# Kernel tuning notes

Measured on AMD Instinct MI355X. Metric: run time of the kernel, lower is better.

## Reference

```python
import jax, jax.numpy as jnp
import numpy as np

D_MODEL, D_K, D_V, N_HEADS = 1024, 64, 64, 16
B, S = 4, 2048


def setup_inputs() -> dict:
    key = jax.random.key(0)
    ks = jax.random.split(key, 11)
    sd = 0.02
    return {
        "q": jax.random.normal(ks[0], (B, S, D_MODEL), jnp.float32),
        "k": jax.random.normal(ks[1], (B, S, D_MODEL), jnp.float32),
        "v": jax.random.normal(ks[2], (B, S, D_MODEL), jnp.float32),
        # stacked per-head projection weights (equivalent to n_heads separate nn.Linear)
        "Wq": jax.random.normal(ks[3], (N_HEADS, D_MODEL, D_K), jnp.float32) * sd,
        "bq": jax.random.normal(ks[4], (N_HEADS, D_K), jnp.float32) * sd,
        "Wk": jax.random.normal(ks[5], (N_HEADS, D_MODEL, D_K), jnp.float32) * sd,
        "bk": jax.random.normal(ks[6], (N_HEADS, D_K), jnp.float32) * sd,
        "Wv": jax.random.normal(ks[7], (N_HEADS, D_MODEL, D_V), jnp.float32) * sd,
        "bv": jax.random.normal(ks[8], (N_HEADS, D_V), jnp.float32) * sd,
        "Wo": jax.random.normal(ks[9], (N_HEADS * D_V, D_MODEL), jnp.float32) * sd,
        "bo": jax.random.normal(ks[10], (D_MODEL,), jnp.float32) * sd,
    }


def reference(q, k, v, Wq, bq, Wk, bk, Wv, bv, Wo, bo):
    # Per-head projections, batched over heads: (B,S,D) x (H,D,dk) -> (B,H,S,dk)
    qh = jnp.einsum("bsd,hdk->bhsk", q, Wq) + bq[None, :, None, :]
    kh = jnp.einsum("bsd,hdk->bhsk", k, Wk) + bk[None, :, None, :]
    vh = jnp.einsum("bsd,hdk->bhsk", v, Wv) + bv[None, :, None, :]
    # scaled dot-product attention per head
    scores = jnp.einsum("bhqk,bhsk->bhqs", qh, kh) / jnp.sqrt(jnp.float32(D_K))
    attn = jax.nn.softmax(scores, axis=-1)
    ctx = jnp.einsum("bhqs,bhsv->bhqv", attn, vh)  # (B,H,S,dv)
    # concat heads -> (B,S,H*dv), then output projection
    ctx = jnp.transpose(ctx, (0, 2, 1, 3)).reshape(B, S, N_HEADS * D_V)
    return ctx @ Wo + bo
```

## Files before the change

### kernel.cpp

```cpp
#include <hip/hip_runtime.h>
#include <hip/hip_bf16.h>

#define DM 1024
#define SEQ 2048
#define NB 4
#define NH 16
#define DKV 64

typedef unsigned short u16;
typedef unsigned int u32;
typedef __attribute__((ext_vector_type(8))) short bf16x8;
typedef __attribute__((ext_vector_type(4))) float f32x4;

__device__ __forceinline__ u16 f2bf(float f) {
    union { float f; unsigned u; } x; x.f = f;
    unsigned r = x.u + 0x7fffu + ((x.u >> 16) & 1u);
    return (u16)(r >> 16);
}
__device__ __forceinline__ u16 f2bf1(float f) {
    union { float f; unsigned u; } x; x.f = f;
    return (u16)((x.u + 0x8000u) >> 16);
}
__device__ __forceinline__ u32 pack2bf(float a, float b) {
    union { float f; unsigned u; } xa, xb; xa.f = a; xb.f = b;
    return __builtin_amdgcn_perm(xb.u + 0x8000u, xa.u + 0x8000u, 0x07060302);
}

#define GLDS16(gp, lp) __builtin_amdgcn_global_load_lds( \
    (const __attribute__((address_space(1))) u32*)(const void*)(gp), \
    (__attribute__((address_space(3))) u32*)(void*)(lp), 16, 0, 0)

__global__ __launch_bounds__(256)
void transpose_to_bf16(const float* __restrict__ src, u16* __restrict__ dst,
                       int R, int C, long srcHeadStride, long dstHeadStride) {
    int h = blockIdx.z;
    src += (long)h * srcHeadStride;
    dst += (long)h * dstHeadStride;
    __shared__ float tile[32][33];
    int r0 = blockIdx.y * 32, c0 = blockIdx.x * 32;
    int tc = threadIdx.x & 31, tr = threadIdx.x >> 5;
    for (int j = 0; j < 4; j++) {
        int r = tr + j * 8;
        tile[r][tc] = src[(long)(r0 + r) * C + c0 + tc];
    }
    __syncthreads();
    for (int j = 0; j < 4; j++) {
        int rr = tr + j * 8;
        dst[(long)(c0 + rr) * R + r0 + tc] = f2bf(tile[tc][rr]);
    }
}

__global__ __launch_bounds__(256)
void cvt_f32_bf16(const float* __restrict__ src, u16* __restrict__ dst, int n4) {
    int i = blockIdx.x * 256 + threadIdx.x;
    int stride = gridDim.x * 256;
    for (; i < n4; i += stride) {
        float4 v = ((const float4*)src)[i];
        uint2 o; o.x = pack2bf(v.x, v.y); o.y = pack2bf(v.z, v.w);
        ((uint2*)dst)[i] = o;
    }
}

template<int OUTMODE>
__global__ __launch_bounds__(256)
void gemm_bf16(const u16* __restrict__ A, const u16* __restrict__ Bt,
               const float* __restrict__ bias, void* __restrict__ Cptr) {
    const int bm0 = blockIdx.x * 128;
    const int bn0 = blockIdx.y * 128;
    __shared__ __align__(16) u16 AsL[128 * 64];
    __shared__ __align__(16) u16 BsL[128 * 64];
    const int tid = threadIdx.x;
    const int lane = tid & 63;
    const int wave = tid >> 6;
    const int wm = (wave >> 1) * 64, wn = (wave & 1) * 64;
    const int l15 = lane & 15, quad = lane >> 4;

    f32x4 acc[4][4];
    for (int i = 0; i < 4; i++) for (int j = 0; j < 4; j++) acc[i][j] = (f32x4)0.0f;

    int rr[4], cc[4];
    for (int j = 0; j < 4; j++) {
        int ci = (wave * 4 + j) * 64 + lane;
        rr[j] = ci >> 3;
        cc[j] = (ci & 7) ^ (rr[j] & 7);
    }
    const int swz = l15 & 7;

    for (int kk = 0; kk < DM; kk += 64) {
        for (int j = 0; j < 4; j++)
            GLDS16(A + (size_t)(bm0 + rr[j]) * DM + kk + cc[j] * 8, AsL + (wave * 4 + j) * 512);
        for (int j = 0; j < 4; j++)
            GLDS16(Bt + (size_t)(bn0 + rr[j]) * DM + kk + cc[j] * 8, BsL + (wave * 4 + j) * 512);
        __syncthreads();
        for (int ks = 0; ks < 2; ks++) {
            bf16x8 a[4], b[4];
            const int fo = ((ks * 4 + quad) ^ swz) * 8;
            for (int mi = 0; mi < 4; mi++)
                a[mi] = *(const bf16x8*)&AsL[(wm + mi * 16 + l15) * 64 + fo];
            for (int ni = 0; ni < 4; ni++)
                b[ni] = *(const bf16x8*)&BsL[(wn + ni * 16 + l15) * 64 + fo];
            for (int mi = 0; mi < 4; mi++)
                for (int ni = 0; ni < 4; ni++)
                    acc[mi][ni] = __builtin_amdgcn_mfma_f32_16x16x32_bf16(a[mi], b[ni], acc[mi][ni], 0, 0, 0);
        }
        __syncthreads();
    }
    for (int mi = 0; mi < 4; mi++) {
        for (int ni = 0; ni < 4; ni++) {
            int n = bn0 + wn + ni * 16 + l15;
            float bb = bias[n];
            int m0 = bm0 + wm + mi * 16 + quad * 4;
            float v0 = acc[mi][ni][0] + bb, v1 = acc[mi][ni][1] + bb;
            float v2 = acc[mi][ni][2] + bb, v3 = acc[mi][ni][3] + bb;
            if (OUTMODE == 0) {
                float* C = (float*)Cptr;
                C[(size_t)(m0 + 0) * DM + n] = v0;
                C[(size_t)(m0 + 1) * DM + n] = v1;
                C[(size_t)(m0 + 2) * DM + n] = v2;
                C[(size_t)(m0 + 3) * DM + n] = v3;
            } else if (OUTMODE == 1) {
                u16* C = (u16*)Cptr;
                int b = m0 >> 11, s = m0 & 2047;
                int h = n >> 6, d = n & 63;
                size_t base = (((size_t)(b * NH + h)) * SEQ + s) * DKV + d;
                C[base + 0 * DKV] = f2bf1(v0);
                C[base + 1 * DKV] = f2bf1(v1);
                C[base + 2 * DKV] = f2bf1(v2);
                C[base + 3 * DKV] = f2bf1(v3);
            } else {
                u16* C = (u16*)Cptr;
                int b = m0 >> 11, s = m0 & 2047;
                int h = n >> 6, d = n & 63;
                uint2 pk; pk.x = pack2bf(v0, v1); pk.y = pack2bf(v2, v3);
                *(uint2*)&C[(((size_t)(b * NH + h)) * DKV + d) * SEQ + s] = pk;
            }
        }
    }
}

__global__ __launch_bounds__(256)
void attn_kernel(const u16* __restrict__ qh, const u16* __restrict__ kh,
                 const u16* __restrict__ vt, u16* __restrict__ ctx) {
    const int qblk = blockIdx.x;
    const int h = blockIdx.y;
    const int b = blockIdx.z;
    const int tid = threadIdx.x;
    const int lane = tid & 63;
    const int wave = tid >> 6;
    const int l15 = lane & 15, quad = lane >> 4;
    const size_t headoff = ((size_t)(b * NH + h)) * SEQ * DKV;
    const u16* Q = qh + headoff;
    const u16* K = kh + headoff;
    const u16* V = vt + headoff;
    const int q0 = qblk * 128 + wave * 32;

    __shared__ __align__(16) u16 KsL[64 * 64];
    __shared__ __align__(16) u16 VtL[64 * 64];
    __shared__ __align__(16) u16 Ps[4][32][80];

    bf16x8 aq[2][2];
    for (int ni = 0; ni < 2; ni++)
        for (int ks = 0; ks < 2; ks++)
            aq[ni][ks] = *(const bf16x8*)&Q[(size_t)(q0 + ni * 16 + l15) * DKV + ks * 32 + quad * 8];

    f32x4 ot[4][2];
    for (int di = 0; di < 4; di++) for (int ni = 0; ni < 2; ni++) ot[di][ni] = (f32x4)0.0f;
    float l_[2] = {0.0f, 0.0f};

    const float sc = 0.125f * 1.44269504088896f;

    int rr[2], cc[2];
    for (int j = 0; j < 2; j++) {
        int ci = (wave * 2 + j) * 64 + lane;
        rr[j] = ci >> 3;
        cc[j] = (ci & 7) ^ (rr[j] & 7);
    }
    const int swz = l15 & 7;

    for (int kv0 = 0; kv0 < SEQ; kv0 += 64) {
        for (int j = 0; j < 2; j++) {
            GLDS16(K + (size_t)(kv0 + rr[j]) * DKV + cc[j] * 8, KsL + (wave * 2 + j) * 512);
            GLDS16(V + (size_t)rr[j] * SEQ + kv0 + cc[j] * 8, VtL + (wave * 2 + j) * 512);
        }
        __syncthreads();

        f32x4 st[4][2];
        for (int mi = 0; mi < 4; mi++) for (int ni = 0; ni < 2; ni++) st[mi][ni] = (f32x4)0.0f;
        for (int ks = 0; ks < 2; ks++) {
            const int fo = ((ks * 4 + quad) ^ swz) * 8;
            bf16x8 bk[4];
            for (int mi = 0; mi < 4; mi++)
                bk[mi] = *(const bf16x8*)&KsL[(mi * 16 + l15) * 64 + fo];
            for (int mi = 0; mi < 4; mi++)
                for (int ni = 0; ni < 2; ni++)
                    st[mi][ni] = __builtin_amdgcn_mfma_f32_16x16x32_bf16(bk[mi], aq[ni][ks], st[mi][ni], 0, 0, 0);
        }

        for (int ni = 0; ni < 2; ni++) {
            float rs = 0.0f;
            for (int mi = 0; mi < 4; mi++) {
                f32x4 p;
                p.x = exp2f(st[mi][ni].x * sc);
                p.y = exp2f(st[mi][ni].y * sc);
                p.z = exp2f(st[mi][ni].z * sc);
                p.w = exp2f(st[mi][ni].w * sc);
                rs += (p.x + p.y) + (p.z + p.w);
                uint2 pk; pk.x = pack2bf(p.x, p.y); pk.y = pack2bf(p.z, p.w);
                *(uint2*)&Ps[wave][ni * 16 + l15][mi * 16 + quad * 4] = pk;
            }
            rs += __shfl_xor(rs, 16);
            rs += __shfl_xor(rs, 32);
            l_[ni] += rs;
        }
        __threadfence_block();

        for (int ks = 0; ks < 2; ks++) {
            const int fo = ((ks * 4 + quad) ^ swz) * 8;
            bf16x8 av[4], bp[2];
            for (int di = 0; di < 4; di++)
                av[di] = *(const bf16x8*)&VtL[(di * 16 + l15) * 64 + fo];
            for (int ni = 0; ni < 2; ni++)
                bp[ni] = *(const bf16x8*)&Ps[wave][ni * 16 + l15][ks * 32 + quad * 8];
            for (int di = 0; di < 4; di++)
                for (int ni = 0; ni < 2; ni++)
                    ot[di][ni] = __builtin_amdgcn_mfma_f32_16x16x32_bf16(av[di], bp[ni], ot[di][ni], 0, 0, 0);
        }
        __syncthreads();
    }

    for (int ni = 0; ni < 2; ni++) {
        float inv = 1.0f / l_[ni];
        int srow = q0 + ni * 16 + l15;
        for (int di = 0; di < 4; di++) {
            uint2 pk;
            pk.x = pack2bf(ot[di][ni].x * inv, ot[di][ni].y * inv);
            pk.y = pack2bf(ot[di][ni].z * inv, ot[di][ni].w * inv);
            *(uint2*)&ctx[((size_t)b * SEQ + srow) * DM + h * DKV + di * 16 + quad * 4] = pk;
        }
    }
}

extern "C" void kernel_launch(void* const* d_in, const int* in_sizes, int n_in,
                              void* d_out, int out_size, void* d_ws, size_t ws_size,
                              hipStream_t stream) {
    const float* q  = (const float*)d_in[0];
    const float* k  = (const float*)d_in[1];
    const float* v  = (const float*)d_in[2];
    const float* Wq = (const float*)d_in[3];
    const float* bq = (const float*)d_in[4];
    const float* Wk = (const float*)d_in[5];
    const float* bk = (const float*)d_in[6];
    const float* Wv = (const float*)d_in[7];
    const float* bv = (const float*)d_in[8];
    const float* Wo = (const float*)d_in[9];
    const float* bo = (const float*)d_in[10];
    float* out = (float*)d_out;

    char* ws = (char*)d_ws;
    const size_t MB = 1024 * 1024;
    u16* WqT = (u16*)(ws + 0 * MB);
    u16* WkT = (u16*)(ws + 2 * MB);
    u16* WvT = (u16*)(ws + 4 * MB);
    u16* WoT = (u16*)(ws + 6 * MB);
    u16* qh  = (u16*)(ws + 8 * MB);
    u16* kh  = (u16*)(ws + 24 * MB);
    u16* vh  = (u16*)(ws + 40 * MB);
    u16* ctx = (u16*)(ws + 56 * MB);
    u16* cvt = ctx;

    const int n4 = NB * SEQ * DM / 4;

    transpose_to_bf16<<<dim3(2, 32, 16), 256, 0, stream>>>(Wq, WqT, 1024, 64, 1024 * 64, 64 * 1024);
    transpose_to_bf16<<<dim3(2, 32, 16), 256, 0, stream>>>(Wk, WkT, 1024, 64, 1024 * 64, 64 * 1024);
    transpose_to_bf16<<<dim3(2, 32, 16), 256, 0, stream>>>(Wv, WvT, 1024, 64, 1024 * 64, 64 * 1024);
    transpose_to_bf16<<<dim3(32, 32, 1), 256, 0, stream>>>(Wo, WoT, 1024, 1024, 0, 0);

    cvt_f32_bf16<<<dim3(2048), 256, 0, stream>>>(q, cvt, n4);
    gemm_bf16<1><<<dim3(64, 8), 256, 0, stream>>>(cvt, WqT, bq, qh);
    cvt_f32_bf16<<<dim3(2048), 256, 0, stream>>>(k, cvt, n4);
    gemm_bf16<1><<<dim3(64, 8), 256, 0, stream>>>(cvt, WkT, bk, kh);
    cvt_f32_bf16<<<dim3(2048), 256, 0, stream>>>(v, cvt, n4);
    gemm_bf16<2><<<dim3(64, 8), 256, 0, stream>>>(cvt, WvT, bv, vh);

    attn_kernel<<<dim3(16, 16, 4), 256, 0, stream>>>(qh, kh, vh, ctx);

    gemm_bf16<0><<<dim3(64, 8), 256, 0, stream>>>(ctx, WoT, bo, out);
}
```

Measured before the change: 408.9 us.

## Double-buffer LDS tiles, fold softmax scale into Q, compute row sums via MFMA

Both the projection GEMM and the attention kernel now use two LDS buffers, prefetching the next K-tile while the current one is computed, which removes one barrier per iteration. The softmax scale times log2(e) is applied in the Q projection epilogue, so the attention loop no longer multiplies scores. Row sums of P come from an extra MFMA against a vector of bf16 ones instead of shuffle reductions, and the P scratch padding shrinks. The costs are doubled LDS use, which may lower occupancy, and row sums taken from bf16-rounded P rather than fp32 values.

```diff
diff --git a/kernel.cpp b/kernel.cpp
--- a/kernel.cpp
+++ b/kernel.cpp
@@ -64,11 +64,11 @@
 template<int OUTMODE>
 __global__ __launch_bounds__(256)
 void gemm_bf16(const u16* __restrict__ A, const u16* __restrict__ Bt,
-               const float* __restrict__ bias, void* __restrict__ Cptr) {
+               const float* __restrict__ bias, void* __restrict__ Cptr, float cscale) {
     const int bm0 = blockIdx.x * 128;
     const int bn0 = blockIdx.y * 128;
-    __shared__ __align__(16) u16 AsL[128 * 64];
-    __shared__ __align__(16) u16 BsL[128 * 64];
+    __shared__ __align__(16) u16 AsL[2][128 * 64];
+    __shared__ __align__(16) u16 BsL[2][128 * 64];
     const int tid = threadIdx.x;
     const int lane = tid & 63;
     const int wave = tid >> 6;
@@ -86,32 +86,40 @@
     }
     const int swz = l15 & 7;
 
+    for (int j = 0; j < 4; j++)
+        GLDS16(A + (size_t)(bm0 + rr[j]) * DM + cc[j] * 8, &AsL[0][(wave * 4 + j) * 512]);
+    for (int j = 0; j < 4; j++)
+        GLDS16(Bt + (size_t)(bn0 + rr[j]) * DM + cc[j] * 8, &BsL[0][(wave * 4 + j) * 512]);
+
+    int buf = 0;
     for (int kk = 0; kk < DM; kk += 64) {
-        for (int j = 0; j < 4; j++)
-            GLDS16(A + (size_t)(bm0 + rr[j]) * DM + kk + cc[j] * 8, AsL + (wave * 4 + j) * 512);
-        for (int j = 0; j < 4; j++)
-            GLDS16(Bt + (size_t)(bn0 + rr[j]) * DM + kk + cc[j] * 8, BsL + (wave * 4 + j) * 512);
         __syncthreads();
+        if (kk + 64 < DM) {
+            for (int j = 0; j < 4; j++)
+                GLDS16(A + (size_t)(bm0 + rr[j]) * DM + kk + 64 + cc[j] * 8, &AsL[buf ^ 1][(wave * 4 + j) * 512]);
+            for (int j = 0; j < 4; j++)
+                GLDS16(Bt + (size_t)(bn0 + rr[j]) * DM + kk + 64 + cc[j] * 8, &BsL[buf ^ 1][(wave * 4 + j) * 512]);
+        }
         for (int ks = 0; ks < 2; ks++) {
             bf16x8 a[4], b[4];
             const int fo = ((ks * 4 + quad) ^ swz) * 8;
             for (int mi = 0; mi < 4; mi++)
-                a[mi] = *(const bf16x8*)&AsL[(wm + mi * 16 + l15) * 64 + fo];
+                a[mi] = *(const bf16x8*)&AsL[buf][(wm + mi * 16 + l15) * 64 + fo];
             for (int ni = 0; ni < 4; ni++)
-                b[ni] = *(const bf16x8*)&BsL[(wn + ni * 16 + l15) * 64 + fo];
+                b[ni] = *(const bf16x8*)&BsL[buf][(wn + ni * 16 + l15) * 64 + fo];
             for (int mi = 0; mi < 4; mi++)
                 for (int ni = 0; ni < 4; ni++)
                     acc[mi][ni] = __builtin_amdgcn_mfma_f32_16x16x32_bf16(a[mi], b[ni], acc[mi][ni], 0, 0, 0);
         }
-        __syncthreads();
+        buf ^= 1;
     }
     for (int mi = 0; mi < 4; mi++) {
         for (int ni = 0; ni < 4; ni++) {
             int n = bn0 + wn + ni * 16 + l15;
             float bb = bias[n];
             int m0 = bm0 + wm + mi * 16 + quad * 4;
-            float v0 = acc[mi][ni][0] + bb, v1 = acc[mi][ni][1] + bb;
-            float v2 = acc[mi][ni][2] + bb, v3 = acc[mi][ni][3] + bb;
+            float v0 = (acc[mi][ni][0] + bb) * cscale, v1 = (acc[mi][ni][1] + bb) * cscale;
+            float v2 = (acc[mi][ni][2] + bb) * cscale, v3 = (acc[mi][ni][3] + bb) * cscale;
             if (OUTMODE == 0) {
                 float* C = (float*)Cptr;
                 C[(size_t)(m0 + 0) * DM + n] = v0;
@@ -154,20 +162,22 @@
     const u16* V = vt + headoff;
     const int q0 = qblk * 128 + wave * 32;
 
-    __shared__ __align__(16) u16 KsL[64 * 64];
-    __shared__ __align__(16) u16 VtL[64 * 64];
-    __shared__ __align__(16) u16 Ps[4][32][80];
+    __shared__ __align__(16) u16 KsL[2][64 * 64];
+    __shared__ __align__(16) u16 VtL[2][64 * 64];
+    __shared__ __align__(16) u16 Ps[4][32][72];
 
     bf16x8 aq[2][2];
     for (int ni = 0; ni < 2; ni++)
         for (int ks = 0; ks < 2; ks++)
             aq[ni][ks] = *(const bf16x8*)&Q[(size_t)(q0 + ni * 16 + l15) * DKV + ks * 32 + quad * 8];
 
+    bf16x8 vones;
+    for (int j = 0; j < 8; j++) vones[j] = (short)0x3F80;
+
     f32x4 ot[4][2];
     for (int di = 0; di < 4; di++) for (int ni = 0; ni < 2; ni++) ot[di][ni] = (f32x4)0.0f;
-    float l_[2] = {0.0f, 0.0f};
-
-    const float sc = 0.125f * 1.44269504088896f;
+    f32x4 lacc[2];
+    lacc[0] = (f32x4)0.0f; lacc[1] = (f32x4)0.0f;
 
     int rr[2], cc[2];
     for (int j = 0; j < 2; j++) {
@@ -177,12 +187,21 @@
     }
     const int swz = l15 & 7;
 
+    for (int j = 0; j < 2; j++) {
+        GLDS16(K + (size_t)rr[j] * DKV + cc[j] * 8, &KsL[0][(wave * 2 + j) * 512]);
+        GLDS16(V + (size_t)rr[j] * SEQ + cc[j] * 8, &VtL[0][(wave * 2 + j) * 512]);
+    }
+
+    int buf = 0;
     for (int kv0 = 0; kv0 < SEQ; kv0 += 64) {
-        for (int j = 0; j < 2; j++) {
-            GLDS16(K + (size_t)(kv0 + rr[j]) * DKV + cc[j] * 8, KsL + (wave * 2 + j) * 512);
-            GLDS16(V + (size_t)rr[j] * SEQ + kv0 + cc[j] * 8, VtL + (wave * 2 + j) * 512);
-        }
         __syncthreads();
+        if (kv0 + 64 < SEQ) {
+            int nx = kv0 + 64;
+            for (int j = 0; j < 2; j++) {
+                GLDS16(K + (size_t)(nx + rr[j]) * DKV + cc[j] * 8, &KsL[buf ^ 1][(wave * 2 + j) * 512]);
+                GLDS16(V + (size_t)rr[j] * SEQ + nx + cc[j] * 8, &VtL[buf ^ 1][(wave * 2 + j) * 512]);
+            }
+        }
 
         f32x4 st[4][2];
         for (int mi = 0; mi < 4; mi++) for (int ni = 0; ni < 2; ni++) st[mi][ni] = (f32x4)0.0f;
@@ -190,27 +209,22 @@
             const int fo = ((ks * 4 + quad) ^ swz) * 8;
             bf16x8 bk[4];
             for (int mi = 0; mi < 4; mi++)
-                bk[mi] = *(const bf16x8*)&KsL[(mi * 16 + l15) * 64 + fo];
+                bk[mi] = *(const bf16x8*)&KsL[buf][(mi * 16 + l15) * 64 + fo];
             for (int mi = 0; mi < 4; mi++)
                 for (int ni = 0; ni < 2; ni++)
                     st[mi][ni] = __builtin_amdgcn_mfma_f32_16x16x32_bf16(bk[mi], aq[ni][ks], st[mi][ni], 0, 0, 0);
         }
 
         for (int ni = 0; ni < 2; ni++) {
-            float rs = 0.0f;
             for (int mi = 0; mi < 4; mi++) {
                 f32x4 p;
-                p.x = exp2f(st[mi][ni].x * sc);
-                p.y = exp2f(st[mi][ni].y * sc);
-                p.z = exp2f(st[mi][ni].z * sc);
-                p.w = exp2f(st[mi][ni].w * sc);
-                rs += (p.x + p.y) + (p.z + p.w);
+                p.x = exp2f(st[mi][ni].x);
+                p.y = exp2f(st[mi][ni].y);
+                p.z = exp2f(st[mi][ni].z);
+                p.w = exp2f(st[mi][ni].w);
                 uint2 pk; pk.x = pack2bf(p.x, p.y); pk.y = pack2bf(p.z, p.w);
                 *(uint2*)&Ps[wave][ni * 16 + l15][mi * 16 + quad * 4] = pk;
             }
-            rs += __shfl_xor(rs, 16);
-            rs += __shfl_xor(rs, 32);
-            l_[ni] += rs;
         }
         __threadfence_block();
 
@@ -218,18 +232,20 @@
             const int fo = ((ks * 4 + quad) ^ swz) * 8;
             bf16x8 av[4], bp[2];
             for (int di = 0; di < 4; di++)
-                av[di] = *(const bf16x8*)&VtL[(di * 16 + l15) * 64 + fo];
+                av[di] = *(const bf16x8*)&VtL[buf][(di * 16 + l15) * 64 + fo];
             for (int ni = 0; ni < 2; ni++)
                 bp[ni] = *(const bf16x8*)&Ps[wave][ni * 16 + l15][ks * 32 + quad * 8];
             for (int di = 0; di < 4; di++)
                 for (int ni = 0; ni < 2; ni++)
                     ot[di][ni] = __builtin_amdgcn_mfma_f32_16x16x32_bf16(av[di], bp[ni], ot[di][ni], 0, 0, 0);
-        }
-        __syncthreads();
+            for (int ni = 0; ni < 2; ni++)
+                lacc[ni] = __builtin_amdgcn_mfma_f32_16x16x32_bf16(vones, bp[ni], lacc[ni], 0, 0, 0);
+        }
+        buf ^= 1;
     }
 
     for (int ni = 0; ni < 2; ni++) {
-        float inv = 1.0f / l_[ni];
+        float inv = 1.0f / lacc[ni][0];
         int srow = q0 + ni * 16 + l15;
         for (int di = 0; di < 4; di++) {
             uint2 pk;
@@ -269,6 +285,7 @@
     u16* cvt = ctx;
 
     const int n4 = NB * SEQ * DM / 4;
+    const float SC = 0.125f * 1.44269504088896f;
 
     transpose_to_bf16<<<dim3(2, 32, 16), 256, 0, stream>>>(Wq, WqT, 1024, 64, 1024 * 64, 64 * 1024);
     transpose_to_bf16<<<dim3(2, 32, 16), 256, 0, stream>>>(Wk, WkT, 1024, 64, 1024 * 64, 64 * 1024);
@@ -276,13 +293,13 @@
     transpose_to_bf16<<<dim3(32, 32, 1), 256, 0, stream>>>(Wo, WoT, 1024, 1024, 0, 0);
 
     cvt_f32_bf16<<<dim3(2048), 256, 0, stream>>>(q, cvt, n4);
-    gemm_bf16<1><<<dim3(64, 8), 256, 0, stream>>>(cvt, WqT, bq, qh);
+    gemm_bf16<1><<<dim3(64, 8), 256, 0, stream>>>(cvt, WqT, bq, qh, SC);
     cvt_f32_bf16<<<dim3(2048), 256, 0, stream>>>(k, cvt, n4);
-    gemm_bf16<1><<<dim3(64, 8), 256, 0, stream>>>(cvt, WkT, bk, kh);
+    gemm_bf16<1><<<dim3(64, 8), 256, 0, stream>>>(cvt, WkT, bk, kh, 1.0f);
     cvt_f32_bf16<<<dim3(2048), 256, 0, stream>>>(v, cvt, n4);
-    gemm_bf16<2><<<dim3(64, 8), 256, 0, stream>>>(cvt, WvT, bv, vh);
+    gemm_bf16<2><<<dim3(64, 8), 256, 0, stream>>>(cvt, WvT, bv, vh, 1.0f);
 
     attn_kernel<<<dim3(16, 16, 4), 256, 0, stream>>>(qh, kh, vh, ctx);
 
-    gemm_bf16<0><<<dim3(64, 8), 256, 0, stream>>>(ctx, WoT, bo, out);
-}
+    gemm_bf16<0><<<dim3(64, 8), 256, 0, stream>>>(ctx, WoT, bo, out, 1.0f);
+}
```

Result: faster. 382.9 us (-6.3%).
